# Performance work log

Hardware: AMD Instinct MI355X
Metric: run time of the kernel (lower is better)

Reference implementation:

```python
import jax, jax.numpy as jnp
import numpy as np

B, S, E, H = 2, 2048, 1024, 16
D = E // H  # head_dim = 64
SPARSE_RATIO = 0.125


def setup_inputs() -> dict:
    key = jax.random.key(0)
    ks = jax.random.split(key, 9)
    def lin(k):
        return jax.random.normal(k, (E, E), dtype=jnp.float32) * 0.02
    return {
        'x': jax.random.normal(ks[0], (B, S, E), dtype=jnp.float32),
        'Wq': lin(ks[1]), 'bq': jnp.zeros((E,), jnp.float32),
        'Wk': lin(ks[2]), 'bk': jnp.zeros((E,), jnp.float32),
        'Wv': lin(ks[3]), 'bv': jnp.zeros((E,), jnp.float32),
        'Wo': lin(ks[4]), 'bo': jnp.zeros((E,), jnp.float32),
    }


def reference(x, Wq, bq, Wk, bk, Wv, bv, Wo, bo):
    # QKV projections: (B,S,E) -> (B,H,S,D)
    def heads(y):
        return y.reshape(B, S, H, D).transpose(0, 2, 1, 3)
    q = heads(x @ Wq.T + bq)
    k = heads(x @ Wk.T + bk)
    v = heads(x @ Wv.T + bv)

    # full score matrix (B,H,S,S), scaled by sqrt(head_dim)
    scores = jnp.einsum('bhsd,bhtd->bhst', q, k) / jnp.sqrt(jnp.float32(D))

    # top-k sparsification applied to scores (fill -inf), then softmax
    top_k = int(SPARSE_RATIO * S)  # 256
    top_vals, top_idx = jax.lax.top_k(scores, top_k)
    neg_inf = jnp.float32(-jnp.inf)
    sparse_scores = jnp.full_like(scores, neg_inf)
    sparse_scores = jnp.put_along_axis(sparse_scores, top_idx, top_vals, axis=-1, inplace=False)

    attn = jax.nn.softmax(sparse_scores, axis=-1)
    out = jnp.einsum('bhst,bhtd->bhsd', attn, v)  # (B,H,S,D)
    out = out.transpose(0, 2, 1, 3).reshape(B, S, E)
    return out @ Wo.T + bo
```

## Files before the change

### kernel.cpp

```cpp
#include <hip/hip_runtime.h>

#define S_LEN 2048
#define NH 16
#define HD 64
#define NBH 32
#define TOPK 256

typedef __bf16 bf16x8_t __attribute__((ext_vector_type(8)));
typedef float  f32x4_t  __attribute__((ext_vector_type(4)));

__device__ __forceinline__ unsigned short rne_bf16(float f) {
    const unsigned x = __float_as_uint(f);
    return (unsigned short)((x + 0x7FFFu + ((x >> 16) & 1u)) >> 16);
}

__global__ __launch_bounds__(256)
void decompose_bf16(const float* __restrict__ in, unsigned short* __restrict__ hi,
                    unsigned short* __restrict__ lo, int n4)
{
    const int i = blockIdx.x * 256 + threadIdx.x;
    if (i >= n4) return;
    const float4 v = reinterpret_cast<const float4*>(in)[i];
    const float f[4] = {v.x, v.y, v.z, v.w};
    unsigned short h[4], l[4];
    #pragma unroll
    for (int j = 0; j < 4; ++j) {
        h[j] = rne_bf16(f[j]);
        const float r = f[j] - __uint_as_float((unsigned)h[j] << 16);
        l[j] = rne_bf16(r);
    }
    reinterpret_cast<ushort4*>(hi)[i] = make_ushort4(h[0], h[1], h[2], h[3]);
    reinterpret_cast<ushort4*>(lo)[i] = make_ushort4(l[0], l[1], l[2], l[3]);
}

__global__ __launch_bounds__(256)
void gemm_mfma_bt(const unsigned short* __restrict__ Ah, const unsigned short* __restrict__ Al,
                  const unsigned short* __restrict__ Bh, const unsigned short* __restrict__ Bl,
                  const float* __restrict__ bias, float* __restrict__ C,
                  unsigned short* __restrict__ Ch, unsigned short* __restrict__ Cl,
                  int M, int N, int K, int mode, int ldc)
{
    __shared__ unsigned short Ash[128][40];
    __shared__ unsigned short Asl[128][40];
    __shared__ unsigned short Bsh[128][40];
    __shared__ unsigned short Bsl[128][40];

    const int tid  = threadIdx.x;
    const int wid  = tid >> 6, lane = tid & 63;
    const int m0   = blockIdx.y * 128, n0 = blockIdx.x * 128;
    const int wr   = (wid >> 1) * 64, wc = (wid & 1) * 64;
    const int r16  = lane & 15, ksub = (lane >> 4) * 8;
    const int srow = tid >> 1;
    const int skb  = (tid & 1) * 16;

    f32x4_t acc[4][4] = {};

    const size_t aBase = (size_t)(m0 + srow) * K + skb;
    const size_t bBase = (size_t)(n0 + srow) * K + skb;

    for (int k0 = 0; k0 < K; k0 += 32) {
        const uint4 a0 = *reinterpret_cast<const uint4*>(&Ah[aBase + k0]);
        const uint4 a1 = *reinterpret_cast<const uint4*>(&Ah[aBase + k0 + 8]);
        const uint4 a2 = *reinterpret_cast<const uint4*>(&Al[aBase + k0]);
        const uint4 a3 = *reinterpret_cast<const uint4*>(&Al[aBase + k0 + 8]);
        const uint4 b0 = *reinterpret_cast<const uint4*>(&Bh[bBase + k0]);
        const uint4 b1 = *reinterpret_cast<const uint4*>(&Bh[bBase + k0 + 8]);
        const uint4 b2 = *reinterpret_cast<const uint4*>(&Bl[bBase + k0]);
        const uint4 b3 = *reinterpret_cast<const uint4*>(&Bl[bBase + k0 + 8]);
        __syncthreads();
        *reinterpret_cast<uint4*>(&Ash[srow][skb])     = a0;
        *reinterpret_cast<uint4*>(&Ash[srow][skb + 8]) = a1;
        *reinterpret_cast<uint4*>(&Asl[srow][skb])     = a2;
        *reinterpret_cast<uint4*>(&Asl[srow][skb + 8]) = a3;
        *reinterpret_cast<uint4*>(&Bsh[srow][skb])     = b0;
        *reinterpret_cast<uint4*>(&Bsh[srow][skb + 8]) = b1;
        *reinterpret_cast<uint4*>(&Bsl[srow][skb])     = b2;
        *reinterpret_cast<uint4*>(&Bsl[srow][skb + 8]) = b3;
        __syncthreads();

        bf16x8_t fah[4], fal[4], fbh[4], fbl[4];
        #pragma unroll
        for (int i = 0; i < 4; ++i) {
            fah[i] = *reinterpret_cast<const bf16x8_t*>(&Ash[wr + i * 16 + r16][ksub]);
            fal[i] = *reinterpret_cast<const bf16x8_t*>(&Asl[wr + i * 16 + r16][ksub]);
        }
        #pragma unroll
        for (int j = 0; j < 4; ++j) {
            fbh[j] = *reinterpret_cast<const bf16x8_t*>(&Bsh[wc + j * 16 + r16][ksub]);
            fbl[j] = *reinterpret_cast<const bf16x8_t*>(&Bsl[wc + j * 16 + r16][ksub]);
        }
        #pragma unroll
        for (int i = 0; i < 4; ++i)
            #pragma unroll
            for (int j = 0; j < 4; ++j) {
                acc[i][j] = __builtin_amdgcn_mfma_f32_16x16x32_bf16(fah[i], fbh[j], acc[i][j], 0, 0, 0);
                acc[i][j] = __builtin_amdgcn_mfma_f32_16x16x32_bf16(fah[i], fbl[j], acc[i][j], 0, 0, 0);
                acc[i][j] = __builtin_amdgcn_mfma_f32_16x16x32_bf16(fal[i], fbh[j], acc[i][j], 0, 0, 0);
            }
    }

    #pragma unroll
    for (int j = 0; j < 4; ++j) {
        const int col = n0 + wc + j * 16 + r16;
        const float bv = bias ? bias[col] : 0.0f;
        #pragma unroll
        for (int i = 0; i < 4; ++i) {
            #pragma unroll
            for (int r = 0; r < 4; ++r) {
                const int row = m0 + wr + i * 16 + (lane >> 4) * 4 + r;
                const float val = acc[i][j][r] + bv;
                if (mode == 0) {
                    C[(size_t)row * ldc + col] = val;
                } else {
                    const int b = row >> 11, s = row & (S_LEN - 1);
                    const int h = col >> 6,  d = col & (HD - 1);
                    const size_t idx = (((size_t)(b * NH + h)) * S_LEN + s) * HD + d;
                    if (mode == 1) {
                        C[idx] = val;
                    } else {
                        const unsigned short hh = rne_bf16(val);
                        Ch[idx] = hh;
                        Cl[idx] = rne_bf16(val - __uint_as_float((unsigned)hh << 16));
                    }
                }
            }
        }
    }
}

__global__ __launch_bounds__(256)
void gemm_score_mfma(const unsigned short* __restrict__ Qh, const unsigned short* __restrict__ Ql,
                     const unsigned short* __restrict__ Kh, const unsigned short* __restrict__ Kl,
                     float* __restrict__ S)
{
    __shared__ unsigned short pl[4][128 * 64];

    const int tid  = threadIdx.x;
    const int wid  = tid >> 6, lane = tid & 63;
    const int m0   = blockIdx.y * 128, n0 = blockIdx.x * 128;
    const int wr   = (wid >> 1) * 64, wc = (wid & 1) * 64;
    const int r16  = lane & 15, ko = (lane >> 4) * 8;
    const size_t headOff = (size_t)blockIdx.z * S_LEN * HD;
    S += (size_t)blockIdx.z * S_LEN * S_LEN;

    {
        const int row = tid >> 1, cs = (tid & 1) * 32;
        const size_t gq = headOff + (size_t)(m0 + row) * HD + cs;
        const size_t gk = headOff + (size_t)(n0 + row) * HD + cs;
        const unsigned short* srcs[4] = {Qh + gq, Ql + gq, Kh + gk, Kl + gk};
        #pragma unroll
        for (int p = 0; p < 4; ++p) {
            #pragma unroll
            for (int j = 0; j < 4; ++j) {
                const uint4 v = *reinterpret_cast<const uint4*>(&srcs[p][j * 8]);
                const int idx = (row * 64 + cs + j * 8) ^ ((row & 7) << 3);
                *reinterpret_cast<uint4*>(&pl[p][idx]) = v;
            }
        }
    }
    __syncthreads();

    f32x4_t acc[4][4] = {};
    #pragma unroll
    for (int ks = 0; ks < 2; ++ks) {
        bf16x8_t fah[4], fal[4], fbh[4], fbl[4];
        #pragma unroll
        for (int i = 0; i < 4; ++i) {
            const int row = wr + i * 16 + r16;
            const int idx = (row * 64 + ko + ks * 32) ^ ((row & 7) << 3);
            fah[i] = *reinterpret_cast<const bf16x8_t*>(&pl[0][idx]);
            fal[i] = *reinterpret_cast<const bf16x8_t*>(&pl[1][idx]);
        }
        #pragma unroll
        for (int j = 0; j < 4; ++j) {
            const int row = wc + j * 16 + r16;
            const int idx = (row * 64 + ko + ks * 32) ^ ((row & 7) << 3);
            fbh[j] = *reinterpret_cast<const bf16x8_t*>(&pl[2][idx]);
            fbl[j] = *reinterpret_cast<const bf16x8_t*>(&pl[3][idx]);
        }
        #pragma unroll
        for (int i = 0; i < 4; ++i)
            #pragma unroll
            for (int j = 0; j < 4; ++j) {
                acc[i][j] = __builtin_amdgcn_mfma_f32_16x16x32_bf16(fah[i], fbh[j], acc[i][j], 0, 0, 0);
                acc[i][j] = __builtin_amdgcn_mfma_f32_16x16x32_bf16(fah[i], fbl[j], acc[i][j], 0, 0, 0);
                acc[i][j] = __builtin_amdgcn_mfma_f32_16x16x32_bf16(fal[i], fbh[j], acc[i][j], 0, 0, 0);
                acc[i][j] = __builtin_amdgcn_mfma_f32_16x16x32_bf16(fal[i], fbl[j], acc[i][j], 0, 0, 0);
            }
    }

    #pragma unroll
    for (int j = 0; j < 4; ++j) {
        const int col = n0 + wc + j * 16 + r16;
        #pragma unroll
        for (int i = 0; i < 4; ++i)
            #pragma unroll
            for (int r = 0; r < 4; ++r) {
                const int row = m0 + wr + i * 16 + (lane >> 4) * 4 + r;
                S[(size_t)row * S_LEN + col] = acc[i][j][r] * 0.125f;
            }
    }
}

__device__ __forceinline__ float wredf_add(float v) {
    #pragma unroll
    for (int m = 32; m > 0; m >>= 1) v += __shfl_xor(v, m, 64);
    return v;
}

#define HCOPY_STRIDE 272
#define HWAVE_WORDS 768

__global__ __launch_bounds__(256, 4)
void topk_softmax_pv(const float* __restrict__ scores, const float* __restrict__ V,
                     float* __restrict__ att, int bh0)
{
    const int wave = threadIdx.x >> 6;
    const int lane = threadIdx.x & 63;
    const int bh   = bh0 + blockIdx.y;
    const int row  = blockIdx.x * 4 + wave;

    const float* srow = scores + (size_t)blockIdx.y * S_LEN * S_LEN + (size_t)row * S_LEN;

    unsigned u[32];
    unsigned mxu = 0u;
    #pragma unroll
    for (int c = 0; c < 8; ++c) {
        const float4 v4 = *reinterpret_cast<const float4*>(&srow[c * 256 + lane * 4]);
        const float f[4] = {v4.x, v4.y, v4.z, v4.w};
        #pragma unroll
        for (int i = 0; i < 4; ++i) {
            const unsigned b = __float_as_uint(f[i]);
            const unsigned k = (b & 0x80000000u) ? ~b : (b | 0x80000000u);
            u[c * 4 + i] = k;
            mxu = k > mxu ? k : mxu;
        }
    }
    #pragma unroll
    for (int m = 32; m > 0; m >>= 1) {
        const unsigned o = (unsigned)__shfl_xor((int)mxu, m, 64);
        mxu = o > mxu ? o : mxu;
    }
    const float mx = __uint_as_float((mxu & 0x80000000u) ? (mxu & 0x7FFFFFFFu) : ~mxu);

    __shared__ unsigned hist[4][HWAVE_WORDS];
    unsigned* const histw = hist[wave];
    unsigned* const myh   = histw + (lane & 1) * HCOPY_STRIDE;

    unsigned prefix = 0;
    int kRem = TOPK;
    unsigned count_eq = 0;

    auto radix_round = [&](int r, bool masked) {
        #pragma unroll
        for (int j = 0; j < 3; ++j)
            *reinterpret_cast<uint4*>(&histw[4 * (lane + 64 * j)]) = make_uint4(0u, 0u, 0u, 0u);
        asm volatile("s_waitcnt lgkmcnt(0)" ::: "memory");
        const int sh = 24 - 8 * r;
        const int ps = 32 - 8 * r;
        #pragma unroll
        for (int i = 0; i < 32; ++i) {
            const unsigned dig = (u[i] >> sh) & 0xFFu;
            if (!masked) {
                atomicAdd(&myh[dig], 1u);
            } else {
                if ((u[i] >> ps) == prefix) atomicAdd(&myh[dig], 1u);
            }
        }
        asm volatile("s_waitcnt lgkmcnt(0)" ::: "memory");
        const uint4 q0 = *reinterpret_cast<const uint4*>(&histw[0 * HCOPY_STRIDE + 4 * lane]);
        const uint4 q1 = *reinterpret_cast<const uint4*>(&histw[1 * HCOPY_STRIDE + 4 * lane]);
        const unsigned c0 = q0.x + q1.x;
        const unsigned c1 = q0.y + q1.y;
        const unsigned c2 = q0.z + q1.z;
        const unsigned c3 = q0.w + q1.w;
        const unsigned cnt = c0 + c1 + c2 + c3;
        unsigned sfx = cnt;
        #pragma unroll
        for (int dd = 1; dd < 64; dd <<= 1) {
            const unsigned t = __shfl_down(sfx, dd, 64);
            if (lane + dd < 64) sfx += t;
        }
        const unsigned g3 = sfx - cnt;
        const unsigned g2 = g3 + c3;
        const unsigned g1 = g2 + c2;
        const unsigned g0 = g1 + c1;
        const unsigned kr = (unsigned)kRem;
        int myd = -1; unsigned mygt = 0, myc = 0;
        if      (g3 < kr && g3 + c3 >= kr) { myd = 4*lane+3; mygt = g3; myc = c3; }
        else if (g2 < kr && g2 + c2 >= kr) { myd = 4*lane+2; mygt = g2; myc = c2; }
        else if (g1 < kr && g1 + c1 >= kr) { myd = 4*lane+1; mygt = g1; myc = c1; }
        else if (g0 < kr && g0 + c0 >= kr) { myd = 4*lane+0; mygt = g0; myc = c0; }
        const unsigned long long bal = __ballot(myd >= 0);
        const int src = __ffsll((unsigned long long)bal) - 1;
        const int d   = __shfl(myd, src, 64);
        kRem    -= __shfl((int)mygt, src, 64);
        count_eq = (unsigned)__shfl((int)myc, src, 64);
        prefix = (prefix << 8) | (unsigned)d;
    };

    radix_round(0, false);
    radix_round(1, true);

    unsigned tau;
    bool takeAll;
    if ((unsigned)kRem == count_eq) {
        tau = prefix << 16;
        takeAll = true;
    } else {
        radix_round(2, true);
        radix_round(3, true);
        tau = prefix;
        takeAll = ((unsigned)kRem == count_eq);
    }
    const int quota = kRem;

    const unsigned long long below = (1ull << lane) - 1ull;
    unsigned incbits = 0u;
    if (takeAll) {
        #pragma unroll
        for (int i = 0; i < 32; ++i)
            if (u[i] >= tau) incbits |= (1u << i);
    } else {
        int prev = 0;
        #pragma unroll
        for (int c = 0; c < 8; ++c) {
            unsigned long long bl[4];
            #pragma unroll
            for (int i = 0; i < 4; ++i) bl[i] = __ballot(u[c * 4 + i] == tau);
            const int below_all = __popcll(bl[0] & below) + __popcll(bl[1] & below)
                                + __popcll(bl[2] & below) + __popcll(bl[3] & below);
            int own = 0;
            #pragma unroll
            for (int i = 0; i < 4; ++i) {
                const bool tie = (u[c * 4 + i] == tau);
                const bool inc = (u[c * 4 + i] > tau) ||
                                 (tie && (prev + below_all + own) < quota);
                own += tie ? 1 : 0;
                if (inc) incbits |= (1u << (c * 4 + i));
            }
            prev += __popcll(bl[0]) + __popcll(bl[1]) + __popcll(bl[2]) + __popcll(bl[3]);
        }
    }

    __shared__ unsigned long long ltw[4][TOPK];
    float ds = 0.f;
    int base = 0;
    #pragma unroll
    for (int c = 0; c < 8; ++c) {
        #pragma unroll
        for (int i = 0; i < 4; ++i) {
            const int id = c * 4 + i;
            const bool inc = ((incbits >> id) & 1u) != 0u;
            const unsigned long long bmask = __ballot(inc);
            float wv = 0.f;
            if (inc) {
                const unsigned uu = u[id];
                const unsigned bb = (uu & 0x80000000u) ? (uu & 0x7FFFFFFFu) : ~uu;
                wv = __expf(__uint_as_float(bb) - mx);
                const int pos = base + __popcll(bmask & below);
                ltw[wave][pos] = ((unsigned long long)__float_as_uint(wv) << 32)
                               | (unsigned)(c * 256 + lane * 4 + i);
            }
            ds += wv;
            base += __popcll(bmask);
        }
    }
    const float inv = 1.0f / wredf_add(ds);
    asm volatile("s_waitcnt lgkmcnt(0)" ::: "memory");

    const float* vh = V + (size_t)bh * S_LEN * HD;
    float a0 = 0.f, a1 = 0.f, a2 = 0.f, a3 = 0.f;
    for (int idx = 0; idx < TOPK; idx += 4) {
        const unsigned long long e0 = ltw[wave][idx + 0];
        const unsigned long long e1 = ltw[wave][idx + 1];
        const unsigned long long e2 = ltw[wave][idx + 2];
        const unsigned long long e3 = ltw[wave][idx + 3];
        a0 = fmaf(__uint_as_float((unsigned)(e0 >> 32)), vh[(((unsigned)e0) << 6) + lane], a0);
        a1 = fmaf(__uint_as_float((unsigned)(e1 >> 32)), vh[(((unsigned)e1) << 6) + lane], a1);
        a2 = fmaf(__uint_as_float((unsigned)(e2 >> 32)), vh[(((unsigned)e2) << 6) + lane], a2);
        a3 = fmaf(__uint_as_float((unsigned)(e3 >> 32)), vh[(((unsigned)e3) << 6) + lane], a3);
    }

    const int b = bh >> 4, h = bh & 15;
    att[(((size_t)b * S_LEN + row) * NH + h) * HD + lane] = ((a0 + a1) + (a2 + a3)) * inv;
}

extern "C" void kernel_launch(void* const* d_in, const int* in_sizes, int n_in,
                              void* d_out, int out_size, void* d_ws, size_t ws_size,
                              hipStream_t stream)
{
    const float* x  = (const float*)d_in[0];
    const float* Wq = (const float*)d_in[1];
    const float* bq = (const float*)d_in[2];
    const float* Wk = (const float*)d_in[3];
    const float* bk = (const float*)d_in[4];
    const float* Wv = (const float*)d_in[5];
    const float* bv = (const float*)d_in[6];
    const float* Wo = (const float*)d_in[7];
    const float* bo = (const float*)d_in[8];
    float* out = (float*)d_out;

    const size_t SD       = (size_t)S_LEN * HD;
    const size_t qkvElems = (size_t)NBH * SD;
    const size_t wElems   = 1024u * 1024u;

    float* v_ws = (float*)d_ws;
    float* attb = v_ws + qkvElems;
    unsigned short* xh  = (unsigned short*)(attb + qkvElems);
    unsigned short* xl  = xh + qkvElems;
    unsigned short* wqh = xl + qkvElems;
    unsigned short* wql = wqh + wElems;
    unsigned short* wkh = wql + wElems;
    unsigned short* wkl = wkh + wElems;
    unsigned short* wvh = wkl + wElems;
    unsigned short* wvl = wvh + wElems;
    unsigned short* woh = wvl + wElems;
    unsigned short* wol = woh + wElems;
    unsigned short* qh  = wol + wElems;
    unsigned short* ql  = qh + qkvElems;
    unsigned short* kh  = ql + qkvElems;
    unsigned short* kl  = kh + qkvElems;
    float* sc = (float*)(kl + qkvElems);

    const size_t scorePerHead = (size_t)S_LEN * S_LEN;
    const size_t fixedBytes = 2 * qkvElems * sizeof(float)
                            + (6 * qkvElems + 8 * wElems) * sizeof(unsigned short);
    size_t availHeads = 0;
    if (ws_size > fixedBytes)
        availHeads = (ws_size - fixedBytes) / (scorePerHead * sizeof(float));
    int hc = (int)(availHeads < 1 ? 1 : (availHeads > (size_t)NBH ? (size_t)NBH : availHeads));
    if (hc > 8) hc = 8;

    const dim3 blk(256);

    decompose_bf16<<<dim3(4096), blk, 0, stream>>>(x,  xh,  xl,  (int)(qkvElems / 4));
    decompose_bf16<<<dim3(1024), blk, 0, stream>>>(Wq, wqh, wql, (int)(wElems / 4));
    decompose_bf16<<<dim3(1024), blk, 0, stream>>>(Wk, wkh, wkl, (int)(wElems / 4));
    decompose_bf16<<<dim3(1024), blk, 0, stream>>>(Wv, wvh, wvl, (int)(wElems / 4));
    decompose_bf16<<<dim3(1024), blk, 0, stream>>>(Wo, woh, wol, (int)(wElems / 4));

    gemm_mfma_bt<<<dim3(8, 32), blk, 0, stream>>>(xh, xl, wqh, wql, bq, nullptr, qh, ql, 4096, 1024, 1024, 2, 0);
    gemm_mfma_bt<<<dim3(8, 32), blk, 0, stream>>>(xh, xl, wkh, wkl, bk, nullptr, kh, kl, 4096, 1024, 1024, 2, 0);
    gemm_mfma_bt<<<dim3(8, 32), blk, 0, stream>>>(xh, xl, wvh, wvl, bv, v_ws, nullptr, nullptr, 4096, 1024, 1024, 1, 0);

    for (int bh0 = 0; bh0 < NBH; bh0 += hc) {
        const int h = (bh0 + hc <= NBH) ? hc : (NBH - bh0);
        gemm_score_mfma<<<dim3(16, 16, h), blk, 0, stream>>>(
            qh + (size_t)bh0 * SD, ql + (size_t)bh0 * SD,
            kh + (size_t)bh0 * SD, kl + (size_t)bh0 * SD, sc);
        topk_softmax_pv<<<dim3(512, h), blk, 0, stream>>>(sc, v_ws, attb, bh0);
    }

    decompose_bf16<<<dim3(4096), blk, 0, stream>>>(attb, xh, xl, (int)(qkvElems / 4));
    gemm_mfma_bt<<<dim3(8, 32), blk, 0, stream>>>(xh, xl, woh, wol, bo, out, nullptr, nullptr, 4096, 1024, 1024, 0, 1024);
}
```

Baseline: 713.7 us.

## Fuse score GEMM with top-k softmax and PV to avoid materializing scores

```diff
diff --git a/kernel.cpp b/kernel.cpp
--- a/kernel.cpp
+++ b/kernel.cpp
@@ -5,6 +5,8 @@
 #define HD 64
 #define NBH 32
 #define TOPK 256
+#define KT 128
+#define NT 16
 
 typedef __bf16 bf16x8_t __attribute__((ext_vector_type(8)));
 typedef float  f32x4_t  __attribute__((ext_vector_type(4)));
@@ -12,6 +14,11 @@
 __device__ __forceinline__ unsigned short rne_bf16(float f) {
     const unsigned x = __float_as_uint(f);
     return (unsigned short)((x + 0x7FFFu + ((x >> 16) & 1u)) >> 16);
+}
+__device__ __forceinline__ float wredf_add(float v) {
+    #pragma unroll
+    for (int m = 32; m > 0; m >>= 1) v += __shfl_xor(v, m, 64);
+    return v;
 }
 
 __global__ __launch_bounds__(256)
@@ -128,262 +135,250 @@
     }
 }
 
-__global__ __launch_bounds__(256)
-void gemm_score_mfma(const unsigned short* __restrict__ Qh, const unsigned short* __restrict__ Ql,
-                     const unsigned short* __restrict__ Kh, const unsigned short* __restrict__ Kl,
-                     float* __restrict__ S)
-{
-    __shared__ unsigned short pl[4][128 * 64];
-
-    const int tid  = threadIdx.x;
-    const int wid  = tid >> 6, lane = tid & 63;
-    const int m0   = blockIdx.y * 128, n0 = blockIdx.x * 128;
-    const int wr   = (wid >> 1) * 64, wc = (wid & 1) * 64;
-    const int r16  = lane & 15, ko = (lane >> 4) * 8;
-    const size_t headOff = (size_t)blockIdx.z * S_LEN * HD;
-    S += (size_t)blockIdx.z * S_LEN * S_LEN;
-
-    {
-        const int row = tid >> 1, cs = (tid & 1) * 32;
-        const size_t gq = headOff + (size_t)(m0 + row) * HD + cs;
-        const size_t gk = headOff + (size_t)(n0 + row) * HD + cs;
-        const unsigned short* srcs[4] = {Qh + gq, Ql + gq, Kh + gk, Kl + gk};
-        #pragma unroll
-        for (int p = 0; p < 4; ++p) {
-            #pragma unroll
-            for (int j = 0; j < 4; ++j) {
-                const uint4 v = *reinterpret_cast<const uint4*>(&srcs[p][j * 8]);
-                const int idx = (row * 64 + cs + j * 8) ^ ((row & 7) << 3);
-                *reinterpret_cast<uint4*>(&pl[p][idx]) = v;
-            }
-        }
-    }
-    __syncthreads();
-
-    f32x4_t acc[4][4] = {};
-    #pragma unroll
-    for (int ks = 0; ks < 2; ++ks) {
-        bf16x8_t fah[4], fal[4], fbh[4], fbl[4];
-        #pragma unroll
-        for (int i = 0; i < 4; ++i) {
-            const int row = wr + i * 16 + r16;
-            const int idx = (row * 64 + ko + ks * 32) ^ ((row & 7) << 3);
-            fah[i] = *reinterpret_cast<const bf16x8_t*>(&pl[0][idx]);
-            fal[i] = *reinterpret_cast<const bf16x8_t*>(&pl[1][idx]);
-        }
-        #pragma unroll
-        for (int j = 0; j < 4; ++j) {
-            const int row = wc + j * 16 + r16;
-            const int idx = (row * 64 + ko + ks * 32) ^ ((row & 7) << 3);
-            fbh[j] = *reinterpret_cast<const bf16x8_t*>(&pl[2][idx]);
-            fbl[j] = *reinterpret_cast<const bf16x8_t*>(&pl[3][idx]);
-        }
-        #pragma unroll
-        for (int i = 0; i < 4; ++i)
-            #pragma unroll
-            for (int j = 0; j < 4; ++j) {
-                acc[i][j] = __builtin_amdgcn_mfma_f32_16x16x32_bf16(fah[i], fbh[j], acc[i][j], 0, 0, 0);
-                acc[i][j] = __builtin_amdgcn_mfma_f32_16x16x32_bf16(fah[i], fbl[j], acc[i][j], 0, 0, 0);
-                acc[i][j] = __builtin_amdgcn_mfma_f32_16x16x32_bf16(fal[i], fbh[j], acc[i][j], 0, 0, 0);
-                acc[i][j] = __builtin_amdgcn_mfma_f32_16x16x32_bf16(fal[i], fbl[j], acc[i][j], 0, 0, 0);
-            }
-    }
-
-    #pragma unroll
-    for (int j = 0; j < 4; ++j) {
-        const int col = n0 + wc + j * 16 + r16;
-        #pragma unroll
-        for (int i = 0; i < 4; ++i)
-            #pragma unroll
-            for (int r = 0; r < 4; ++r) {
-                const int row = m0 + wr + i * 16 + (lane >> 4) * 4 + r;
-                S[(size_t)row * S_LEN + col] = acc[i][j][r] * 0.125f;
-            }
-    }
-}
-
-__device__ __forceinline__ float wredf_add(float v) {
-    #pragma unroll
-    for (int m = 32; m > 0; m >>= 1) v += __shfl_xor(v, m, 64);
-    return v;
-}
-
 #define HCOPY_STRIDE 272
 #define HWAVE_WORDS 768
 
-__global__ __launch_bounds__(256, 4)
-void topk_softmax_pv(const float* __restrict__ scores, const float* __restrict__ V,
-                     float* __restrict__ att, int bh0)
+struct LdsA {
+    unsigned short qh[16][72], ql[16][72];
+    unsigned short kh[KT][72], kl[KT][72];
+    float sb[2][16][132];
+};
+struct LdsB {
+    unsigned hist[8][HWAVE_WORDS];
+    unsigned long long ltw[16][TOPK];
+};
+union FusedLDS { LdsA a; LdsB b; };
+
+__global__ __launch_bounds__(512, 4)
+void fused_score_topk_pv(const unsigned short* __restrict__ Qh, const unsigned short* __restrict__ Ql,
+                         const unsigned short* __restrict__ Kh, const unsigned short* __restrict__ Kl,
+                         const float* __restrict__ V, float* __restrict__ att)
 {
-    const int wave = threadIdx.x >> 6;
-    const int lane = threadIdx.x & 63;
-    const int bh   = bh0 + blockIdx.y;
-    const int row  = blockIdx.x * 4 + wave;
-
-    const float* srow = scores + (size_t)blockIdx.y * S_LEN * S_LEN + (size_t)row * S_LEN;
-
-    unsigned u[32];
-    unsigned mxu = 0u;
+    __shared__ FusedLDS sm;
+    const int tid  = threadIdx.x;
+    const int w    = tid >> 6, lane = tid & 63;
+    const int bh   = blockIdx.y;
+    const int rb   = blockIdx.x;
+    const size_t headOff = (size_t)bh * S_LEN * HD;
+
+    if (tid < 256) {
+        const int plane = tid >> 7;
+        const int t2  = tid & 127;
+        const int row = t2 >> 3, col = (t2 & 7) * 8;
+        const unsigned short* src = (plane ? Ql : Qh) + headOff + (size_t)(rb * 16 + row) * HD + col;
+        const uint4 v = *reinterpret_cast<const uint4*>(src);
+        *reinterpret_cast<uint4*>((plane ? sm.a.ql[row] : sm.a.qh[row]) + col) = v;
+    }
+
+    unsigned u[2][32];
+    unsigned mxu0 = 0u, mxu1 = 0u;
+
     #pragma unroll
-    for (int c = 0; c < 8; ++c) {
-        const float4 v4 = *reinterpret_cast<const float4*>(&srow[c * 256 + lane * 4]);
-        const float f[4] = {v4.x, v4.y, v4.z, v4.w};
-        #pragma unroll
-        for (int i = 0; i < 4; ++i) {
-            const unsigned b = __float_as_uint(f[i]);
+    for (int t = 0; t < NT; ++t) {
+        __syncthreads();
+        #pragma unroll
+        for (int p = 0; p < 2; ++p) {
+            const int e   = (p * 512 + tid) * 8;
+            const int row = e >> 6, col = e & 63;
+            const size_t g = headOff + (size_t)(t * KT + row) * HD + col;
+            const uint4 vh = *reinterpret_cast<const uint4*>(&Kh[g]);
+            const uint4 vl = *reinterpret_cast<const uint4*>(&Kl[g]);
+            *reinterpret_cast<uint4*>(&sm.a.kh[row][col]) = vh;
+            *reinterpret_cast<uint4*>(&sm.a.kl[row][col]) = vl;
+        }
+        __syncthreads();
+
+        f32x4_t acc = {};
+        #pragma unroll
+        for (int ks = 0; ks < 2; ++ks) {
+            const int qrow = lane & 15, ko = (lane >> 4) * 8 + ks * 32;
+            const bf16x8_t fqh = *reinterpret_cast<const bf16x8_t*>(&sm.a.qh[qrow][ko]);
+            const bf16x8_t fql = *reinterpret_cast<const bf16x8_t*>(&sm.a.ql[qrow][ko]);
+            const int krow = w * 16 + (lane & 15);
+            const bf16x8_t fkh = *reinterpret_cast<const bf16x8_t*>(&sm.a.kh[krow][ko]);
+            const bf16x8_t fkl = *reinterpret_cast<const bf16x8_t*>(&sm.a.kl[krow][ko]);
+            acc = __builtin_amdgcn_mfma_f32_16x16x32_bf16(fqh, fkh, acc, 0, 0, 0);
+            acc = __builtin_amdgcn_mfma_f32_16x16x32_bf16(fqh, fkl, acc, 0, 0, 0);
+            acc = __builtin_amdgcn_mfma_f32_16x16x32_bf16(fql, fkh, acc, 0, 0, 0);
+            acc = __builtin_amdgcn_mfma_f32_16x16x32_bf16(fql, fkl, acc, 0, 0, 0);
+        }
+        #pragma unroll
+        for (int r = 0; r < 4; ++r)
+            sm.a.sb[t & 1][(lane >> 4) * 4 + r][w * 16 + (lane & 15)] = acc[r] * 0.125f;
+
+        if (t > 0) {
+            #pragma unroll
+            for (int j = 0; j < 2; ++j) {
+                const int id = (t - 1) * 2 + j;
+                {
+                    const unsigned b = __float_as_uint(sm.a.sb[(t - 1) & 1][2 * w][j * 64 + lane]);
+                    const unsigned k = (b & 0x80000000u) ? ~b : (b | 0x80000000u);
+                    u[0][id] = k; mxu0 = k > mxu0 ? k : mxu0;
+                }
+                {
+                    const unsigned b = __float_as_uint(sm.a.sb[(t - 1) & 1][2 * w + 1][j * 64 + lane]);
+                    const unsigned k = (b & 0x80000000u) ? ~b : (b | 0x80000000u);
+                    u[1][id] = k; mxu1 = k > mxu1 ? k : mxu1;
+                }
+            }
+        }
+    }
+    __syncthreads();
+    #pragma unroll
+    for (int j = 0; j < 2; ++j) {
+        const int id = (NT - 1) * 2 + j;
+        {
+            const unsigned b = __float_as_uint(sm.a.sb[(NT - 1) & 1][2 * w][j * 64 + lane]);
             const unsigned k = (b & 0x80000000u) ? ~b : (b | 0x80000000u);
-            u[c * 4 + i] = k;
-            mxu = k > mxu ? k : mxu;
-        }
-    }
-    #pragma unroll
-    for (int m = 32; m > 0; m >>= 1) {
-        const unsigned o = (unsigned)__shfl_xor((int)mxu, m, 64);
-        mxu = o > mxu ? o : mxu;
-    }
-    const float mx = __uint_as_float((mxu & 0x80000000u) ? (mxu & 0x7FFFFFFFu) : ~mxu);
-
-    __shared__ unsigned hist[4][HWAVE_WORDS];
-    unsigned* const histw = hist[wave];
+            u[0][id] = k; mxu0 = k > mxu0 ? k : mxu0;
+        }
+        {
+            const unsigned b = __float_as_uint(sm.a.sb[(NT - 1) & 1][2 * w + 1][j * 64 + lane]);
+            const unsigned k = (b & 0x80000000u) ? ~b : (b | 0x80000000u);
+            u[1][id] = k; mxu1 = k > mxu1 ? k : mxu1;
+        }
+    }
+    __syncthreads();
+
+    unsigned* const histw = sm.b.hist[w];
     unsigned* const myh   = histw + (lane & 1) * HCOPY_STRIDE;
-
-    unsigned prefix = 0;
-    int kRem = TOPK;
-    unsigned count_eq = 0;
-
-    auto radix_round = [&](int r, bool masked) {
-        #pragma unroll
-        for (int j = 0; j < 3; ++j)
-            *reinterpret_cast<uint4*>(&histw[4 * (lane + 64 * j)]) = make_uint4(0u, 0u, 0u, 0u);
-        asm volatile("s_waitcnt lgkmcnt(0)" ::: "memory");
-        const int sh = 24 - 8 * r;
-        const int ps = 32 - 8 * r;
-        #pragma unroll
-        for (int i = 0; i < 32; ++i) {
-            const unsigned dig = (u[i] >> sh) & 0xFFu;
-            if (!masked) {
-                atomicAdd(&myh[dig], 1u);
-            } else {
-                if ((u[i] >> ps) == prefix) atomicAdd(&myh[dig], 1u);
-            }
-        }
-        asm volatile("s_waitcnt lgkmcnt(0)" ::: "memory");
-        const uint4 q0 = *reinterpret_cast<const uint4*>(&histw[0 * HCOPY_STRIDE + 4 * lane]);
-        const uint4 q1 = *reinterpret_cast<const uint4*>(&histw[1 * HCOPY_STRIDE + 4 * lane]);
-        const unsigned c0 = q0.x + q1.x;
-        const unsigned c1 = q0.y + q1.y;
-        const unsigned c2 = q0.z + q1.z;
-        const unsigned c3 = q0.w + q1.w;
-        const unsigned cnt = c0 + c1 + c2 + c3;
-        unsigned sfx = cnt;
-        #pragma unroll
-        for (int dd = 1; dd < 64; dd <<= 1) {
-            const unsigned t = __shfl_down(sfx, dd, 64);
-            if (lane + dd < 64) sfx += t;
-        }
-        const unsigned g3 = sfx - cnt;
-        const unsigned g2 = g3 + c3;
-        const unsigned g1 = g2 + c2;
-        const unsigned g0 = g1 + c1;
-        const unsigned kr = (unsigned)kRem;
-        int myd = -1; unsigned mygt = 0, myc = 0;
-        if      (g3 < kr && g3 + c3 >= kr) { myd = 4*lane+3; mygt = g3; myc = c3; }
-        else if (g2 < kr && g2 + c2 >= kr) { myd = 4*lane+2; mygt = g2; myc = c2; }
-        else if (g1 < kr && g1 + c1 >= kr) { myd = 4*lane+1; mygt = g1; myc = c1; }
-        else if (g0 < kr && g0 + c0 >= kr) { myd = 4*lane+0; mygt = g0; myc = c0; }
-        const unsigned long long bal = __ballot(myd >= 0);
-        const int src = __ffsll((unsigned long long)bal) - 1;
-        const int d   = __shfl(myd, src, 64);
-        kRem    -= __shfl((int)mygt, src, 64);
-        count_eq = (unsigned)__shfl((int)myc, src, 64);
-        prefix = (prefix << 8) | (unsigned)d;
-    };
-
-    radix_round(0, false);
-    radix_round(1, true);
-
-    unsigned tau;
-    bool takeAll;
-    if ((unsigned)kRem == count_eq) {
-        tau = prefix << 16;
-        takeAll = true;
-    } else {
-        radix_round(2, true);
-        radix_round(3, true);
-        tau = prefix;
-        takeAll = ((unsigned)kRem == count_eq);
-    }
-    const int quota = kRem;
-
     const unsigned long long below = (1ull << lane) - 1ull;
-    unsigned incbits = 0u;
-    if (takeAll) {
-        #pragma unroll
-        for (int i = 0; i < 32; ++i)
-            if (u[i] >= tau) incbits |= (1u << i);
-    } else {
-        int prev = 0;
-        #pragma unroll
-        for (int c = 0; c < 8; ++c) {
-            unsigned long long bl[4];
-            #pragma unroll
-            for (int i = 0; i < 4; ++i) bl[i] = __ballot(u[c * 4 + i] == tau);
-            const int below_all = __popcll(bl[0] & below) + __popcll(bl[1] & below)
-                                + __popcll(bl[2] & below) + __popcll(bl[3] & below);
-            int own = 0;
-            #pragma unroll
-            for (int i = 0; i < 4; ++i) {
-                const bool tie = (u[c * 4 + i] == tau);
-                const bool inc = (u[c * 4 + i] > tau) ||
-                                 (tie && (prev + below_all + own) < quota);
-                own += tie ? 1 : 0;
-                if (inc) incbits |= (1u << (c * 4 + i));
-            }
-            prev += __popcll(bl[0]) + __popcll(bl[1]) + __popcll(bl[2]) + __popcll(bl[3]);
-        }
-    }
-
-    __shared__ unsigned long long ltw[4][TOPK];
-    float ds = 0.f;
-    int base = 0;
-    #pragma unroll
-    for (int c = 0; c < 8; ++c) {
-        #pragma unroll
-        for (int i = 0; i < 4; ++i) {
-            const int id = c * 4 + i;
+    const float* vh = V + headOff;
+    const int bb = bh >> 4, hh = bh & 15;
+
+    auto process_row = [&](const unsigned (&ur)[32], unsigned mxu, int lrow) {
+        #pragma unroll
+        for (int m = 32; m > 0; m >>= 1) {
+            const unsigned o = (unsigned)__shfl_xor((int)mxu, m, 64);
+            mxu = o > mxu ? o : mxu;
+        }
+        const float mx = __uint_as_float((mxu & 0x80000000u) ? (mxu & 0x7FFFFFFFu) : ~mxu);
+
+        unsigned prefix = 0;
+        int kRem = TOPK;
+        unsigned count_eq = 0;
+
+        auto radix_round = [&](int r, bool masked) {
+            #pragma unroll
+            for (int j = 0; j < 3; ++j)
+                *reinterpret_cast<uint4*>(&histw[4 * (lane + 64 * j)]) = make_uint4(0u, 0u, 0u, 0u);
+            asm volatile("s_waitcnt lgkmcnt(0)" ::: "memory");
+            const int sh = 24 - 8 * r;
+            const int ps = 32 - 8 * r;
+            #pragma unroll
+            for (int i = 0; i < 32; ++i) {
+                const unsigned dig = (ur[i] >> sh) & 0xFFu;
+                if (!masked) {
+                    atomicAdd(&myh[dig], 1u);
+                } else {
+                    if ((ur[i] >> ps) == prefix) atomicAdd(&myh[dig], 1u);
+                }
+            }
+            asm volatile("s_waitcnt lgkmcnt(0)" ::: "memory");
+            const uint4 q0 = *reinterpret_cast<const uint4*>(&histw[0 * HCOPY_STRIDE + 4 * lane]);
+            const uint4 q1 = *reinterpret_cast<const uint4*>(&histw[1 * HCOPY_STRIDE + 4 * lane]);
+            const unsigned c0 = q0.x + q1.x;
+            const unsigned c1 = q0.y + q1.y;
+            const unsigned c2 = q0.z + q1.z;
+            const unsigned c3 = q0.w + q1.w;
+            const unsigned cnt = c0 + c1 + c2 + c3;
+            unsigned sfx = cnt;
+            #pragma unroll
+            for (int dd = 1; dd < 64; dd <<= 1) {
+                const unsigned tt = __shfl_down(sfx, dd, 64);
+                if (lane + dd < 64) sfx += tt;
+            }
+            const unsigned g3 = sfx - cnt;
+            const unsigned g2 = g3 + c3;
+            const unsigned g1 = g2 + c2;
+            const unsigned g0 = g1 + c1;
+            const unsigned kr = (unsigned)kRem;
+            int myd = -1; unsigned mygt = 0, myc = 0;
+            if      (g3 < kr && g3 + c3 >= kr) { myd = 4 * lane + 3; mygt = g3; myc = c3; }
+            else if (g2 < kr && g2 + c2 >= kr) { myd = 4 * lane + 2; mygt = g2; myc = c2; }
+            else if (g1 < kr && g1 + c1 >= kr) { myd = 4 * lane + 1; mygt = g1; myc = c1; }
+            else if (g0 < kr && g0 + c0 >= kr) { myd = 4 * lane + 0; mygt = g0; myc = c0; }
+            const unsigned long long bal = __ballot(myd >= 0);
+            const int src = __ffsll((unsigned long long)bal) - 1;
+            const int d   = __shfl(myd, src, 64);
+            kRem    -= __shfl((int)mygt, src, 64);
+            count_eq = (unsigned)__shfl((int)myc, src, 64);
+            prefix = (prefix << 8) | (unsigned)d;
+        };
+
+        radix_round(0, false);
+        radix_round(1, true);
+
+        unsigned tau;
+        bool takeAll;
+        if ((unsigned)kRem == count_eq) {
+            tau = prefix << 16;
+            takeAll = true;
+        } else {
+            radix_round(2, true);
+            radix_round(3, true);
+            tau = prefix;
+            takeAll = ((unsigned)kRem == count_eq);
+        }
+        const int quota = kRem;
+
+        unsigned incbits = 0u;
+        if (takeAll) {
+            #pragma unroll
+            for (int i = 0; i < 32; ++i)
+                if (ur[i] >= tau) incbits |= (1u << i);
+        } else {
+            int prev = 0;
+            #pragma unroll
+            for (int id = 0; id < 32; ++id) {
+                const bool tie = (ur[id] == tau);
+                const unsigned long long bl = __ballot(tie);
+                const int below_cnt = __popcll(bl & below);
+                const bool inc = (ur[id] > tau) || (tie && (prev + below_cnt) < quota);
+                if (inc) incbits |= (1u << id);
+                prev += __popcll(bl);
+            }
+        }
+
+        float ds = 0.f;
+        int base = 0;
+        #pragma unroll
+        for (int id = 0; id < 32; ++id) {
             const bool inc = ((incbits >> id) & 1u) != 0u;
             const unsigned long long bmask = __ballot(inc);
             float wv = 0.f;
             if (inc) {
-                const unsigned uu = u[id];
-                const unsigned bb = (uu & 0x80000000u) ? (uu & 0x7FFFFFFFu) : ~uu;
-                wv = __expf(__uint_as_float(bb) - mx);
+                const unsigned uu = ur[id];
+                const unsigned bbu = (uu & 0x80000000u) ? (uu & 0x7FFFFFFFu) : ~uu;
+                wv = __expf(__uint_as_float(bbu) - mx);
                 const int pos = base + __popcll(bmask & below);
-                ltw[wave][pos] = ((unsigned long long)__float_as_uint(wv) << 32)
-                               | (unsigned)(c * 256 + lane * 4 + i);
+                sm.b.ltw[lrow][pos] = ((unsigned long long)__float_as_uint(wv) << 32)
+                                    | (unsigned)(id * 64 + lane);
             }
             ds += wv;
             base += __popcll(bmask);
         }
-    }
-    const float inv = 1.0f / wredf_add(ds);
-    asm volatile("s_waitcnt lgkmcnt(0)" ::: "memory");
-
-    const float* vh = V + (size_t)bh * S_LEN * HD;
-    float a0 = 0.f, a1 = 0.f, a2 = 0.f, a3 = 0.f;
-    for (int idx = 0; idx < TOPK; idx += 4) {
-        const unsigned long long e0 = ltw[wave][idx + 0];
-        const unsigned long long e1 = ltw[wave][idx + 1];
-        const unsigned long long e2 = ltw[wave][idx + 2];
-        const unsigned long long e3 = ltw[wave][idx + 3];
-        a0 = fmaf(__uint_as_float((unsigned)(e0 >> 32)), vh[(((unsigned)e0) << 6) + lane], a0);
-        a1 = fmaf(__uint_as_float((unsigned)(e1 >> 32)), vh[(((unsigned)e1) << 6) + lane], a1);
-        a2 = fmaf(__uint_as_float((unsigned)(e2 >> 32)), vh[(((unsigned)e2) << 6) + lane], a2);
-        a3 = fmaf(__uint_as_float((unsigned)(e3 >> 32)), vh[(((unsigned)e3) << 6) + lane], a3);
-    }
-
-    const int b = bh >> 4, h = bh & 15;
-    att[(((size_t)b * S_LEN + row) * NH + h) * HD + lane] = ((a0 + a1) + (a2 + a3)) * inv;
+        const float inv = 1.0f / wredf_add(ds);
+        asm volatile("s_waitcnt lgkmcnt(0)" ::: "memory");
+
+        float a0 = 0.f, a1 = 0.f, a2 = 0.f, a3 = 0.f;
+        for (int idx = 0; idx < TOPK; idx += 4) {
+            const unsigned long long e0 = sm.b.ltw[lrow][idx + 0];
+            const unsigned long long e1 = sm.b.ltw[lrow][idx + 1];
+            const unsigned long long e2 = sm.b.ltw[lrow][idx + 2];
+            const unsigned long long e3 = sm.b.ltw[lrow][idx + 3];
+            a0 = fmaf(__uint_as_float((unsigned)(e0 >> 32)), vh[(((unsigned)e0) << 6) + lane], a0);
+            a1 = fmaf(__uint_as_float((unsigned)(e1 >> 32)), vh[(((unsigned)e1) << 6) + lane], a1);
+            a2 = fmaf(__uint_as_float((unsigned)(e2 >> 32)), vh[(((unsigned)e2) << 6) + lane], a2);
+            a3 = fmaf(__uint_as_float((unsigned)(e3 >> 32)), vh[(((unsigned)e3) << 6) + lane], a3);
+        }
+
+        const int grow = rb * 16 + lrow;
+        att[(((size_t)bb * S_LEN + grow) * NH + hh) * HD + lane] = ((a0 + a1) + (a2 + a3)) * inv;
+    };
+
+    process_row(u[0], mxu0, 2 * w);
+    process_row(u[1], mxu1, 2 * w + 1);
 }
 
 extern "C" void kernel_launch(void* const* d_in, const int* in_sizes, int n_in,
@@ -421,16 +416,6 @@
     unsigned short* ql  = qh + qkvElems;
     unsigned short* kh  = ql + qkvElems;
     unsigned short* kl  = kh + qkvElems;
-    float* sc = (float*)(kl + qkvElems);
-
-    const size_t scorePerHead = (size_t)S_LEN * S_LEN;
-    const size_t fixedBytes = 2 * qkvElems * sizeof(float)
-                            + (6 * qkvElems + 8 * wElems) * sizeof(unsigned short);
-    size_t availHeads = 0;
-    if (ws_size > fixedBytes)
-        availHeads = (ws_size - fixedBytes) / (scorePerHead * sizeof(float));
-    int hc = (int)(availHeads < 1 ? 1 : (availHeads > (size_t)NBH ? (size_t)NBH : availHeads));
-    if (hc > 8) hc = 8;
 
     const dim3 blk(256);
 
@@ -444,13 +429,7 @@
     gemm_mfma_bt<<<dim3(8, 32), blk, 0, stream>>>(xh, xl, wkh, wkl, bk, nullptr, kh, kl, 4096, 1024, 1024, 2, 0);
     gemm_mfma_bt<<<dim3(8, 32), blk, 0, stream>>>(xh, xl, wvh, wvl, bv, v_ws, nullptr, nullptr, 4096, 1024, 1024, 1, 0);
 
-    for (int bh0 = 0; bh0 < NBH; bh0 += hc) {
-        const int h = (bh0 + hc <= NBH) ? hc : (NBH - bh0);
-        gemm_score_mfma<<<dim3(16, 16, h), blk, 0, stream>>>(
-            qh + (size_t)bh0 * SD, ql + (size_t)bh0 * SD,
-            kh + (size_t)bh0 * SD, kl + (size_t)bh0 * SD, sc);
-        topk_softmax_pv<<<dim3(512, h), blk, 0, stream>>>(sc, v_ws, attb, bh0);
-    }
+    fused_score_topk_pv<<<dim3(S_LEN / 16, NBH), dim3(512), 0, stream>>>(qh, ql, kh, kl, v_ws, attb);
 
     decompose_bf16<<<dim3(4096), blk, 0, stream>>>(attb, xh, xl, (int)(qkvElems / 4));
     gemm_mfma_bt<<<dim3(8, 32), blk, 0, stream>>>(xh, xl, woh, wol, bo, out, nullptr, nullptr, 4096, 1024, 1024, 0, 1024);
```

Result: slower. 780.5 us (+9.4%).
